# Optimization experiments

Measured on AMD Instinct MI355X. Metric: run time of the kernel, lower is better.

The kernel has to match this reference:

```python
import jax, jax.numpy as jnp
import numpy as np
import math

Ds = 2048
N = 16384
M = 1024


def setup_inputs() -> dict:
    key = jax.random.key(0)
    kD, kS, kW = jax.random.split(key, 3)
    D = jax.random.normal(kD, (N, Ds), dtype=jnp.float32)
    S = jax.random.normal(kS, (M, Ds), dtype=jnp.float32)
    W = jax.random.normal(kW, (Ds, Ds), dtype=jnp.float32) * 0.01  # init.normal std=0.01
    return {"D": D, "S": S, "W": W}


def reference(D, S, W):
    ds = D.shape[1]
    temperature = 1.0
    # cross-attention: [n, m]
    scores = (D @ S.T) / (math.sqrt(ds) * temperature)
    att_weight = jax.nn.softmax(scores, axis=1)
    att_S = att_weight @ S  # [n, Ds]
    # bilinear per row: logits[i] = D[i] . (W @ att_S[i])  -> fused einsum
    logits = jnp.einsum('nd,de,ne->n', D, W, att_S)
    log_prob = jnp.sum(jax.nn.log_sigmoid(logits))
    return log_prob
```

## Files before the change

kernel.cpp:

```cpp
#include <hip/hip_runtime.h>
#include <stdint.h>

typedef unsigned short u16;
typedef unsigned int u32;
typedef __attribute__((ext_vector_type(8))) short bf16x8;
typedef __attribute__((ext_vector_type(4))) float f32x4;

#define DS 2048
#define NROWS 16384
#define MS 1024
#define K2 2048

__device__ __forceinline__ u16 f2bf(float f) {
  u32 u = __float_as_uint(f);
  u32 r = (u + 0x7fffu + ((u >> 16) & 1u)) >> 16;
  return (u16)r;
}
__device__ __forceinline__ float bf2f(u16 h) {
  return __uint_as_float(((u32)h) << 16);
}

__global__ __launch_bounds__(256) void k_conv(const float* __restrict__ in,
                                              u16* __restrict__ out, int n4) {
  int i = blockIdx.x * blockDim.x + threadIdx.x;
  int stride = gridDim.x * blockDim.x;
  for (; i < n4; i += stride) {
    float4 v = ((const float4*)in)[i];
    ushort4 o;
    o.x = f2bf(v.x); o.y = f2bf(v.y); o.z = f2bf(v.z); o.w = f2bf(v.w);
    ((ushort4*)out)[i] = o;
  }
}

__global__ __launch_bounds__(256) void k_conv_S(const float* __restrict__ in,
                                                u16* __restrict__ Sbf,
                                                u16* __restrict__ Bt, int n4) {
  int i = blockIdx.x * blockDim.x + threadIdx.x;
  int stride = gridDim.x * blockDim.x;
  for (; i < n4; i += stride) {
    float4 v = ((const float4*)in)[i];
    ushort4 o;
    o.x = f2bf(v.x); o.y = f2bf(v.y); o.z = f2bf(v.z); o.w = f2bf(v.w);
    ((ushort4*)Sbf)[i] = o;
    int m = i >> 9;
    int c4 = i & 511;
    ((ushort4*)Bt)[(size_t)m * 1024 + c4] = o;
  }
}

__device__ __forceinline__ void gload16(const u16* g, u16* l) {
  __builtin_amdgcn_global_load_lds(
      (const __attribute__((address_space(1))) void*)g,
      (__attribute__((address_space(3))) void*)l, 16, 0, 0);
}

__global__ __launch_bounds__(256, 2) void k_gemm_bt(const u16* __restrict__ A,
                                                    const u16* __restrict__ Bt,
                                                    u16* __restrict__ C, int ldc,
                                                    int M, int N, int K) {
  __shared__ u16 lsA[128 * 32];
  __shared__ u16 lsB[128 * 32];
  const int tid = threadIdx.x;
  const int wid = tid >> 6;
  const int lane = tid & 63;
  const int brow = blockIdx.y * 128;
  const int bcol = blockIdx.x * 128;
  const int wm = wid >> 1;
  const int wn = wid & 1;

  f32x4 zero = {0.f, 0.f, 0.f, 0.f};
  f32x4 acc[4][4];
#pragma unroll
  for (int i = 0; i < 4; ++i)
#pragma unroll
    for (int j = 0; j < 4; ++j) acc[i][j] = zero;

  const int srow = lane >> 2;
  const int skoct = (lane & 3) * 8;
  const u16* gA = A + (size_t)(brow + wid * 32 + srow) * K + skoct;
  const u16* gB = Bt + (size_t)(bcol + wid * 32 + srow) * K + skoct;
  u16* lA0 = &lsA[(wid * 32) * 32];
  u16* lA1 = &lsA[(wid * 32 + 16) * 32];
  u16* lB0 = &lsB[(wid * 32) * 32];
  u16* lB1 = &lsB[(wid * 32 + 16) * 32];
  const size_t row16 = (size_t)16 * K;

  const int arow = wm * 64 + (lane & 15);
  const int bcr = wn * 64 + (lane & 15);
  const int koff = (lane >> 4) * 8;

  for (int kt = 0; kt < K; kt += 32) {
    gload16(gA + kt, lA0);
    gload16(gA + kt + row16, lA1);
    gload16(gB + kt, lB0);
    gload16(gB + kt + row16, lB1);
    __syncthreads();

    bf16x8 af[4], bfr[4];
#pragma unroll
    for (int i = 0; i < 4; ++i) af[i] = *(const bf16x8*)&lsA[(arow + i * 16) * 32 + koff];
#pragma unroll
    for (int i = 0; i < 4; ++i) bfr[i] = *(const bf16x8*)&lsB[(bcr + i * 16) * 32 + koff];
#pragma unroll
    for (int mi = 0; mi < 4; ++mi)
#pragma unroll
      for (int ni = 0; ni < 4; ++ni)
        acc[mi][ni] = __builtin_amdgcn_mfma_f32_16x16x32_bf16(af[mi], bfr[ni],
                                                              acc[mi][ni], 0, 0, 0);
    __syncthreads();
  }

  const int crow0 = brow + wm * 64 + (lane >> 4) * 4;
  const int ccol0 = bcol + wn * 64 + (lane & 15);
#pragma unroll
  for (int mi = 0; mi < 4; ++mi)
#pragma unroll
    for (int ni = 0; ni < 4; ++ni)
#pragma unroll
      for (int r = 0; r < 4; ++r)
        C[(size_t)(crow0 + mi * 16 + r) * ldc + (ccol0 + ni * 16)] = f2bf(acc[mi][ni][r]);
}

#define SINV 0.022097086912079608f

#define DSR(dst, addr) asm volatile("ds_read_b128 %0, %1" : "=v"(dst) : "v"(addr))

#define AADDR(B, QM, MI, KK) \
  ((abase + (B) * 65536u + (QM) * 16384u + (MI) * 2048u) ^ ((KK) * 64u))
#define BADDR(B, QN, NI, KK) \
  ((bbase + (B) * 65536u + (QN) * 16384u + (NI) * 2048u) ^ ((KK) * 64u))

#define STG(gptr, b, AB, h, kt)                                                     \
  do {                                                                              \
    gload16(gptr + (size_t)((h) * 128) * K2 + (kt),                                 \
            &lds[(b) * 32768 + (AB) * 16384 + (h) * 8192 + wid * 512]);             \
    gload16(gptr + (size_t)((h) * 128 + 64) * K2 + (kt),                            \
            &lds[(b) * 32768 + (AB) * 16384 + (h) * 8192 + 4096 + wid * 512]);      \
  } while (0)
#define STG_A(b, h, kt) STG(gAs, b, 0, h, kt)
#define STG_B(b, h, kt) STG(gBs, b, 1, h, kt)

#define RD_ALPHA(B)                                                   \
  do {                                                                \
    _Pragma("unroll") for (int mi = 0; mi < 4; ++mi) {                \
      DSR(af[mi][0], AADDR(B, 0, mi, 0));                             \
      DSR(af[mi][1], AADDR(B, 0, mi, 1));                             \
    }                                                                 \
    _Pragma("unroll") for (int ni = 0; ni < 2; ++ni) {                \
      DSR(bq[0][ni][0], BADDR(B, 0, ni, 0));                          \
      DSR(bq[0][ni][1], BADDR(B, 0, ni, 1));                          \
    }                                                                 \
  } while (0)
#define RD_BETA(B)                                                    \
  do {                                                                \
    _Pragma("unroll") for (int ni = 0; ni < 2; ++ni) {                \
      DSR(bq[1][ni][0], BADDR(B, 1, ni, 0));                          \
      DSR(bq[1][ni][1], BADDR(B, 1, ni, 1));                          \
    }                                                                 \
  } while (0)
#define RD_GAMMA(B)                                                   \
  do {                                                                \
    _Pragma("unroll") for (int mi = 0; mi < 4; ++mi) {                \
      DSR(af[mi][0], AADDR(B, 1, mi, 0));                             \
      DSR(af[mi][1], AADDR(B, 1, mi, 1));                             \
    }                                                                 \
  } while (0)

#define MMAQ(QM, QN)                                                               \
  do {                                                                             \
    _Pragma("unroll") for (int mi = 0; mi < 4; ++mi)                               \
        _Pragma("unroll") for (int ni = 0; ni < 2; ++ni) {                         \
      acc[QM][QN][mi][ni] = __builtin_amdgcn_mfma_f32_16x16x32_bf16(               \
          af[mi][0], bq[QN][ni][0], acc[QM][QN][mi][ni], 0, 0, 0);                 \
      acc[QM][QN][mi][ni] = __builtin_amdgcn_mfma_f32_16x16x32_bf16(               \
          af[mi][1], bq[QN][ni][1], acc[QM][QN][mi][ni], 0, 0, 0);                 \
    }                                                                              \
  } while (0)

#define PH_MID()                                              \
  __builtin_amdgcn_s_barrier();                               \
  asm volatile("s_waitcnt lgkmcnt(0)" ::: "memory");          \
  __builtin_amdgcn_sched_barrier(0);                          \
  __builtin_amdgcn_s_setprio(1)
#define PH_END() __builtin_amdgcn_s_setprio(0)
#define BAR() __builtin_amdgcn_s_barrier()
#define VM6() asm volatile("s_waitcnt vmcnt(6)" ::: "memory")
#define VM0() asm volatile("s_waitcnt vmcnt(0)" ::: "memory")

__global__ __launch_bounds__(512, 2) void k_gemm8(const u16* __restrict__ A,
                                                  const u16* __restrict__ Bt,
                                                  float* __restrict__ Pnd) {
  extern __shared__ u16 lds[];
  const int tid = threadIdx.x;
  const int wid = tid >> 6;
  const int lane = tid & 63;
  const int bid = blockIdx.x;
  const int swz = (bid & 7) * 64 + (bid >> 3);
  const int by = swz >> 3, bx = swz & 7;
  const int brow = by * 256, bcol = bx * 256;
  const int wm = wid >> 2, wn = wid & 3;
  const int l15 = lane & 15, s0 = lane >> 4;

  const int tr = tid >> 3;
  const int scol = ((tid & 7) ^ (tr & 7)) << 3;
  const u16* gAs = A + (size_t)(brow + tr) * K2 + scol;
  const u16* gBs = Bt + (size_t)(bcol + tr) * K2 + scol;

  const u32 lb = (u32)(uintptr_t)(&lds[0]);
  const u32 xorp = ((u32)(s0 ^ (lane & 7))) << 4;
  const u32 abase = lb + ((u32)(wm * 64 + l15) << 7) + xorp;
  const u32 bbase = lb + 32768u + ((u32)(wn * 32 + l15) << 7) + xorp;

  f32x4 acc[2][2][4][2];
#pragma unroll
  for (int a = 0; a < 2; ++a)
#pragma unroll
    for (int b = 0; b < 2; ++b)
#pragma unroll
      for (int c = 0; c < 4; ++c)
#pragma unroll
        for (int d = 0; d < 2; ++d) acc[a][b][c][d] = (f32x4){0.f, 0.f, 0.f, 0.f};

  bf16x8 af[4][2], bq[2][2][2];

  STG_A(0, 0, 0); STG_B(0, 0, 0); STG_B(0, 1, 0); STG_A(0, 1, 0);
  STG_A(1, 0, 64); STG_B(1, 0, 64); STG_B(1, 1, 64);
  VM6();
  BAR();

  int kt0 = 0;
#pragma unroll 1
  for (int j = 0; j < 15; ++j, kt0 += 128) {
    const int kt1 = kt0 + 64, ktn0 = kt0 + 128, ktn1 = kt0 + 192;
    RD_ALPHA(0); STG_A(1, 1, kt1);  PH_MID(); MMAQ(0, 0); PH_END(); BAR();
    RD_BETA(0);  STG_A(0, 0, ktn0); PH_MID(); MMAQ(0, 1); PH_END(); BAR();
    RD_GAMMA(0); STG_B(0, 0, ktn0); PH_MID(); MMAQ(1, 0); PH_END(); BAR();
    STG_B(0, 1, ktn0);              PH_MID(); MMAQ(1, 1); PH_END(); VM6(); BAR();
    RD_ALPHA(1); STG_A(0, 1, ktn0); PH_MID(); MMAQ(0, 0); PH_END(); BAR();
    RD_BETA(1);  STG_A(1, 0, ktn1); PH_MID(); MMAQ(0, 1); PH_END(); BAR();
    RD_GAMMA(1); STG_B(1, 0, ktn1); PH_MID(); MMAQ(1, 0); PH_END(); BAR();
    STG_B(1, 1, ktn1);              PH_MID(); MMAQ(1, 1); PH_END(); VM6(); BAR();
  }
  {
    const int kt1 = kt0 + 64;
    RD_ALPHA(0); STG_A(1, 1, kt1);  PH_MID(); MMAQ(0, 0); PH_END(); BAR();
    RD_BETA(0);                     PH_MID(); MMAQ(0, 1); PH_END(); BAR();
    RD_GAMMA(0);                    PH_MID(); MMAQ(1, 0); PH_END(); BAR();
                                    PH_MID(); MMAQ(1, 1); PH_END(); VM0(); BAR();
    RD_ALPHA(1);                    PH_MID(); MMAQ(0, 0); PH_END(); BAR();
    RD_BETA(1);                     PH_MID(); MMAQ(0, 1); PH_END(); BAR();
    RD_GAMMA(1);                    PH_MID(); MMAQ(1, 0); PH_END(); BAR();
                                    PH_MID(); MMAQ(1, 1); PH_END(); BAR();
  }

  __syncthreads();
  float* red = (float*)&lds[0];

#pragma unroll
  for (int qm = 0; qm < 2; ++qm)
#pragma unroll
    for (int mi = 0; mi < 4; ++mi)
#pragma unroll
      for (int r = 0; r < 4; ++r) {
        float num = 0.f, den = 0.f;
#pragma unroll
        for (int qn = 0; qn < 2; ++qn)
#pragma unroll
          for (int ni = 0; ni < 2; ++ni) {
            float v = acc[qm][qn][mi][ni][r];
            float g = __shfl_xor(v, 1);
            float e = __expf(v * SINV);
            num += e * g;
            den += e;
          }
        num += __shfl_xor(num, 2); den += __shfl_xor(den, 2);
        num += __shfl_xor(num, 4); den += __shfl_xor(den, 4);
        num += __shfl_xor(num, 8); den += __shfl_xor(den, 8);
        if (l15 == 0) {
          int slot = qm * 16 + mi * 4 + r;
          red[((wid * 32 + slot) * 4 + s0) * 2 + 0] = num;
          red[((wid * 32 + slot) * 4 + s0) * 2 + 1] = den;
        }
      }
  __syncthreads();
  {
    int rloc = tid >> 1, which = tid & 1;
    int qm = rloc >> 7, wmr = (rloc >> 6) & 1, mi = (rloc >> 4) & 3;
    int lg = (rloc >> 2) & 3, r = rloc & 3;
    int slot = qm * 16 + mi * 4 + r;
    float v = 0.f;
#pragma unroll
    for (int w2 = 0; w2 < 4; ++w2)
      v += red[(((wmr * 4 + w2) * 32 + slot) * 4 + lg) * 2 + which];
    Pnd[((size_t)(brow + rloc) * 8 + bx) * 2 + which] = v;
  }
}

__global__ __launch_bounds__(256) void k_rowfinal(const float* __restrict__ Pnd,
                                                  float* __restrict__ part) {
  int row = blockIdx.x * 256 + threadIdx.x;
  const float4* p = (const float4*)(Pnd + (size_t)row * 16);
  float num = 0.f, den = 0.f;
#pragma unroll
  for (int i = 0; i < 4; ++i) {
    float4 v = p[i];
    num += v.x + v.z;
    den += v.y + v.w;
  }
  float logit = num / den;
  float ls = (logit >= 0.f) ? -log1pf(__expf(-logit))
                            : (logit - log1pf(__expf(logit)));
  __shared__ float red[4];
#pragma unroll
  for (int off = 32; off > 0; off >>= 1) ls += __shfl_down(ls, off);
  if ((threadIdx.x & 63) == 0) red[threadIdx.x >> 6] = ls;
  __syncthreads();
  if (threadIdx.x == 0) part[blockIdx.x] = red[0] + red[1] + red[2] + red[3];
}

__global__ __launch_bounds__(64) void k_final64(const float* __restrict__ part,
                                                float* __restrict__ out) {
  float v = part[threadIdx.x];
#pragma unroll
  for (int off = 32; off > 0; off >>= 1) v += __shfl_down(v, off);
  if (threadIdx.x == 0) out[0] = v;
}

extern "C" void kernel_launch(void* const* d_in, const int* in_sizes, int n_in,
                              void* d_out, int out_size, void* d_ws, size_t ws_size,
                              hipStream_t stream) {
  const float* D = (const float*)d_in[0];
  const float* S = (const float*)d_in[1];
  const float* W = (const float*)d_in[2];

  char* w = (char*)d_ws;
  u16* Dbf = (u16*)w; w += (size_t)NROWS * DS * 2;
  u16* Bt = (u16*)w;  w += (size_t)DS * DS * 2;
  u16* Wbf = (u16*)w; w += (size_t)DS * DS * 2;
  u16* Sbf = (u16*)w; w += (size_t)MS * DS * 2;
  float* Pnd = (float*)w; w += (size_t)NROWS * 16 * 4;
  float* part = (float*)w;

  (void)hipFuncSetAttribute((const void*)k_gemm8,
                            hipFuncAttributeMaxDynamicSharedMemorySize, 131072);

  k_conv<<<1024, 256, 0, stream>>>(W, Wbf, DS * DS / 4);
  k_conv_S<<<512, 256, 0, stream>>>(S, Sbf, Bt, MS * DS / 4);
  k_conv<<<2048, 256, 0, stream>>>(D, Dbf, NROWS * DS / 4);

  k_gemm_bt<<<dim3(DS / 128, MS / 128), 256, 0, stream>>>(
      Sbf, Wbf, Bt + DS, 2 * DS, MS, DS, DS);

  k_gemm8<<<512, 512, 131072, stream>>>(Dbf, Bt, Pnd);

  k_rowfinal<<<NROWS / 256, 256, 0, stream>>>(Pnd, part);
  k_final64<<<1, 64, 0, stream>>>(part, (float*)d_out);
}
```

Before: 200.9 us.

## Software-pipeline LDS fragment reads in main GEMM and halve small GEMM tile rows

The main k_gemm8 loop is restructured so LDS fragment reads for the next quadrant are issued before the current MFMA batch. Double-buffered register fragments (afA/afB, bq0/bq1) and graded lgkmcnt waits replace the full lgkmcnt(0) wait each phase, so LDS latency can hide behind matrix math, and global stages are reordered with vmcnt(4) waits. Separately, the S·W GEMM uses 64-row tiles to launch twice as many blocks for better CU occupancy. The price is more fragment registers and tighter, hand-tuned wait counts that must match the issue order exactly.

```diff
diff --git a/kernel.cpp b/kernel.cpp
--- a/kernel.cpp
+++ b/kernel.cpp
@@ -54,55 +54,51 @@
       (__attribute__((address_space(3))) void*)l, 16, 0, 0);
 }
 
-__global__ __launch_bounds__(256, 2) void k_gemm_bt(const u16* __restrict__ A,
-                                                    const u16* __restrict__ Bt,
-                                                    u16* __restrict__ C, int ldc,
-                                                    int M, int N, int K) {
-  __shared__ u16 lsA[128 * 32];
+__global__ __launch_bounds__(256, 2) void k_gemm_bt64(const u16* __restrict__ A,
+                                                      const u16* __restrict__ Bt,
+                                                      u16* __restrict__ C, int ldc,
+                                                      int K) {
+  __shared__ u16 lsA[64 * 32];
   __shared__ u16 lsB[128 * 32];
   const int tid = threadIdx.x;
   const int wid = tid >> 6;
   const int lane = tid & 63;
-  const int brow = blockIdx.y * 128;
+  const int brow = blockIdx.y * 64;
   const int bcol = blockIdx.x * 128;
   const int wm = wid >> 1;
   const int wn = wid & 1;
 
-  f32x4 zero = {0.f, 0.f, 0.f, 0.f};
-  f32x4 acc[4][4];
-#pragma unroll
-  for (int i = 0; i < 4; ++i)
-#pragma unroll
-    for (int j = 0; j < 4; ++j) acc[i][j] = zero;
+  f32x4 acc[2][4];
+#pragma unroll
+  for (int i = 0; i < 2; ++i)
+#pragma unroll
+    for (int j = 0; j < 4; ++j) acc[i][j] = (f32x4){0.f, 0.f, 0.f, 0.f};
 
   const int srow = lane >> 2;
   const int skoct = (lane & 3) * 8;
-  const u16* gA = A + (size_t)(brow + wid * 32 + srow) * K + skoct;
+  const u16* gA = A + (size_t)(brow + wid * 16 + srow) * K + skoct;
   const u16* gB = Bt + (size_t)(bcol + wid * 32 + srow) * K + skoct;
-  u16* lA0 = &lsA[(wid * 32) * 32];
-  u16* lA1 = &lsA[(wid * 32 + 16) * 32];
+  u16* lA = &lsA[(wid * 16) * 32];
   u16* lB0 = &lsB[(wid * 32) * 32];
   u16* lB1 = &lsB[(wid * 32 + 16) * 32];
   const size_t row16 = (size_t)16 * K;
 
-  const int arow = wm * 64 + (lane & 15);
+  const int arow = wm * 32 + (lane & 15);
   const int bcr = wn * 64 + (lane & 15);
   const int koff = (lane >> 4) * 8;
 
   for (int kt = 0; kt < K; kt += 32) {
-    gload16(gA + kt, lA0);
-    gload16(gA + kt + row16, lA1);
+    gload16(gA + kt, lA);
     gload16(gB + kt, lB0);
     gload16(gB + kt + row16, lB1);
     __syncthreads();
-
-    bf16x8 af[4], bfr[4];
-#pragma unroll
-    for (int i = 0; i < 4; ++i) af[i] = *(const bf16x8*)&lsA[(arow + i * 16) * 32 + koff];
+    bf16x8 af[2], bfr[4];
+#pragma unroll
+    for (int i = 0; i < 2; ++i) af[i] = *(const bf16x8*)&lsA[(arow + i * 16) * 32 + koff];
 #pragma unroll
     for (int i = 0; i < 4; ++i) bfr[i] = *(const bf16x8*)&lsB[(bcr + i * 16) * 32 + koff];
 #pragma unroll
-    for (int mi = 0; mi < 4; ++mi)
+    for (int mi = 0; mi < 2; ++mi)
 #pragma unroll
       for (int ni = 0; ni < 4; ++ni)
         acc[mi][ni] = __builtin_amdgcn_mfma_f32_16x16x32_bf16(af[mi], bfr[ni],
@@ -110,10 +106,10 @@
     __syncthreads();
   }
 
-  const int crow0 = brow + wm * 64 + (lane >> 4) * 4;
+  const int crow0 = brow + wm * 32 + (lane >> 4) * 4;
   const int ccol0 = bcol + wn * 64 + (lane & 15);
 #pragma unroll
-  for (int mi = 0; mi < 4; ++mi)
+  for (int mi = 0; mi < 2; ++mi)
 #pragma unroll
     for (int ni = 0; ni < 4; ++ni)
 #pragma unroll
@@ -123,69 +119,59 @@
 
 #define SINV 0.022097086912079608f
 
-#define DSR(dst, addr) asm volatile("ds_read_b128 %0, %1" : "=v"(dst) : "v"(addr))
-
-#define AADDR(B, QM, MI, KK) \
-  ((abase + (B) * 65536u + (QM) * 16384u + (MI) * 2048u) ^ ((KK) * 64u))
-#define BADDR(B, QN, NI, KK) \
-  ((bbase + (B) * 65536u + (QN) * 16384u + (NI) * 2048u) ^ ((KK) * 64u))
-
-#define STG(gptr, b, AB, h, kt)                                                     \
-  do {                                                                              \
-    gload16(gptr + (size_t)((h) * 128) * K2 + (kt),                                 \
-            &lds[(b) * 32768 + (AB) * 16384 + (h) * 8192 + wid * 512]);             \
-    gload16(gptr + (size_t)((h) * 128 + 64) * K2 + (kt),                            \
-            &lds[(b) * 32768 + (AB) * 16384 + (h) * 8192 + 4096 + wid * 512]);      \
-  } while (0)
-#define STG_A(b, h, kt) STG(gAs, b, 0, h, kt)
-#define STG_B(b, h, kt) STG(gBs, b, 1, h, kt)
-
-#define RD_ALPHA(B)                                                   \
-  do {                                                                \
-    _Pragma("unroll") for (int mi = 0; mi < 4; ++mi) {                \
-      DSR(af[mi][0], AADDR(B, 0, mi, 0));                             \
-      DSR(af[mi][1], AADDR(B, 0, mi, 1));                             \
-    }                                                                 \
-    _Pragma("unroll") for (int ni = 0; ni < 2; ++ni) {                \
-      DSR(bq[0][ni][0], BADDR(B, 0, ni, 0));                          \
-      DSR(bq[0][ni][1], BADDR(B, 0, ni, 1));                          \
-    }                                                                 \
-  } while (0)
-#define RD_BETA(B)                                                    \
-  do {                                                                \
-    _Pragma("unroll") for (int ni = 0; ni < 2; ++ni) {                \
-      DSR(bq[1][ni][0], BADDR(B, 1, ni, 0));                          \
-      DSR(bq[1][ni][1], BADDR(B, 1, ni, 1));                          \
-    }                                                                 \
-  } while (0)
-#define RD_GAMMA(B)                                                   \
-  do {                                                                \
-    _Pragma("unroll") for (int mi = 0; mi < 4; ++mi) {                \
-      DSR(af[mi][0], AADDR(B, 1, mi, 0));                             \
-      DSR(af[mi][1], AADDR(B, 1, mi, 1));                             \
-    }                                                                 \
-  } while (0)
-
-#define MMAQ(QM, QN)                                                               \
+#define DSR(d, a, IMM) \
+  asm volatile("ds_read_b128 %0, %1 offset:%c2" : "=v"(d) : "v"(a), "n"(IMM))
+
+#define RD_A0(k0, k1, dst)                              \
+  DSR(dst[0][0], k0, 0);     DSR(dst[0][1], k1, 0);     \
+  DSR(dst[1][0], k0, 2048);  DSR(dst[1][1], k1, 2048);  \
+  DSR(dst[2][0], k0, 4096);  DSR(dst[2][1], k1, 4096);  \
+  DSR(dst[3][0], k0, 6144);  DSR(dst[3][1], k1, 6144)
+#define RD_A1(k0, k1, dst)                              \
+  DSR(dst[0][0], k0, 16384); DSR(dst[0][1], k1, 16384); \
+  DSR(dst[1][0], k0, 18432); DSR(dst[1][1], k1, 18432); \
+  DSR(dst[2][0], k0, 20480); DSR(dst[2][1], k1, 20480); \
+  DSR(dst[3][0], k0, 22528); DSR(dst[3][1], k1, 22528)
+#define RD_B0(k0, k1, dst)                              \
+  DSR(dst[0][0], k0, 0);     DSR(dst[0][1], k1, 0);     \
+  DSR(dst[1][0], k0, 2048);  DSR(dst[1][1], k1, 2048)
+#define RD_B1(k0, k1, dst)                              \
+  DSR(dst[0][0], k0, 16384); DSR(dst[0][1], k1, 16384); \
+  DSR(dst[1][0], k0, 18432); DSR(dst[1][1], k1, 18432)
+
+#define MMAQ(AF, BQ, QM, QN)                                                       \
   do {                                                                             \
     _Pragma("unroll") for (int mi = 0; mi < 4; ++mi)                               \
         _Pragma("unroll") for (int ni = 0; ni < 2; ++ni) {                         \
       acc[QM][QN][mi][ni] = __builtin_amdgcn_mfma_f32_16x16x32_bf16(               \
-          af[mi][0], bq[QN][ni][0], acc[QM][QN][mi][ni], 0, 0, 0);                 \
+          AF[mi][0], BQ[ni][0], acc[QM][QN][mi][ni], 0, 0, 0);                     \
       acc[QM][QN][mi][ni] = __builtin_amdgcn_mfma_f32_16x16x32_bf16(               \
-          af[mi][1], bq[QN][ni][1], acc[QM][QN][mi][ni], 0, 0, 0);                 \
+          AF[mi][1], BQ[ni][1], acc[QM][QN][mi][ni], 0, 0, 0);                     \
     }                                                                              \
   } while (0)
 
-#define PH_MID()                                              \
-  __builtin_amdgcn_s_barrier();                               \
-  asm volatile("s_waitcnt lgkmcnt(0)" ::: "memory");          \
-  __builtin_amdgcn_sched_barrier(0);                          \
-  __builtin_amdgcn_s_setprio(1)
-#define PH_END() __builtin_amdgcn_s_setprio(0)
+#define LGKM(N)                                              \
+  asm volatile("s_waitcnt lgkmcnt(" #N ")" ::: "memory");    \
+  __builtin_amdgcn_sched_barrier(0)
+#define VMW(N) asm volatile("s_waitcnt vmcnt(" #N ")" ::: "memory")
+#define PRIO1() __builtin_amdgcn_s_setprio(1)
+#define PRIO0() __builtin_amdgcn_s_setprio(0)
 #define BAR() __builtin_amdgcn_s_barrier()
-#define VM6() asm volatile("s_waitcnt vmcnt(6)" ::: "memory")
-#define VM0() asm volatile("s_waitcnt vmcnt(0)" ::: "memory")
+
+#define STGA(b, h, kt)                                                            \
+  do {                                                                            \
+    gload16(pA + (size_t)((h) * 128) * K2 + (kt),                                 \
+            &lds[(b) * 32768 + (h) * 8192 + wid * 512]);                          \
+    gload16(pA + (size_t)((h) * 128 + 64) * K2 + (kt),                            \
+            &lds[(b) * 32768 + (h) * 8192 + 4096 + wid * 512]);                   \
+  } while (0)
+#define STGB(b, h, kt)                                                            \
+  do {                                                                            \
+    gload16(pB + (size_t)((h) * 128) * K2 + (kt),                                 \
+            &lds[(b) * 32768 + 16384 + (h) * 8192 + wid * 512]);                  \
+    gload16(pB + (size_t)((h) * 128 + 64) * K2 + (kt),                            \
+            &lds[(b) * 32768 + 16384 + (h) * 8192 + 4096 + wid * 512]);           \
+  } while (0)
 
 __global__ __launch_bounds__(512, 2) void k_gemm8(const u16* __restrict__ A,
                                                   const u16* __restrict__ Bt,
@@ -203,13 +189,19 @@
 
   const int tr = tid >> 3;
   const int scol = ((tid & 7) ^ (tr & 7)) << 3;
-  const u16* gAs = A + (size_t)(brow + tr) * K2 + scol;
-  const u16* gBs = Bt + (size_t)(bcol + tr) * K2 + scol;
+  const u16* pA = A + (size_t)(brow + tr) * K2 + scol;
+  const u16* pB = Bt + (size_t)(bcol + tr) * K2 + scol;
 
   const u32 lb = (u32)(uintptr_t)(&lds[0]);
   const u32 xorp = ((u32)(s0 ^ (lane & 7))) << 4;
-  const u32 abase = lb + ((u32)(wm * 64 + l15) << 7) + xorp;
-  const u32 bbase = lb + 32768u + ((u32)(wn * 32 + l15) << 7) + xorp;
+  const u32 aA00 = lb + ((u32)(wm * 64 + l15) << 7) + xorp;
+  const u32 aA01 = aA00 ^ 64u;
+  const u32 aA10 = aA00 + 65536u;
+  const u32 aA11 = aA10 ^ 64u;
+  const u32 aB00 = lb + 32768u + ((u32)(wn * 32 + l15) << 7) + xorp;
+  const u32 aB01 = aB00 ^ 64u;
+  const u32 aB10 = aB00 + 65536u;
+  const u32 aB11 = aB10 ^ 64u;
 
   f32x4 acc[2][2][4][2];
 #pragma unroll
@@ -221,36 +213,61 @@
 #pragma unroll
         for (int d = 0; d < 2; ++d) acc[a][b][c][d] = (f32x4){0.f, 0.f, 0.f, 0.f};
 
-  bf16x8 af[4][2], bq[2][2][2];
-
-  STG_A(0, 0, 0); STG_B(0, 0, 0); STG_B(0, 1, 0); STG_A(0, 1, 0);
-  STG_A(1, 0, 64); STG_B(1, 0, 64); STG_B(1, 1, 64);
-  VM6();
+  bf16x8 afA[4][2], afB[4][2], bq0[2][2], bq1[2][2];
+
+  STGA(0, 0, 0); STGB(0, 0, 0); STGB(0, 1, 0); STGA(0, 1, 0);
+  STGA(1, 0, 64);
+  VMW(2);
   BAR();
-
-  int kt0 = 0;
+  RD_A0(aA00, aA01, afA);
+  RD_B0(aB00, aB01, bq0);
+
+  int kb = 0;
 #pragma unroll 1
-  for (int j = 0; j < 15; ++j, kt0 += 128) {
-    const int kt1 = kt0 + 64, ktn0 = kt0 + 128, ktn1 = kt0 + 192;
-    RD_ALPHA(0); STG_A(1, 1, kt1);  PH_MID(); MMAQ(0, 0); PH_END(); BAR();
-    RD_BETA(0);  STG_A(0, 0, ktn0); PH_MID(); MMAQ(0, 1); PH_END(); BAR();
-    RD_GAMMA(0); STG_B(0, 0, ktn0); PH_MID(); MMAQ(1, 0); PH_END(); BAR();
-    STG_B(0, 1, ktn0);              PH_MID(); MMAQ(1, 1); PH_END(); VM6(); BAR();
-    RD_ALPHA(1); STG_A(0, 1, ktn0); PH_MID(); MMAQ(0, 0); PH_END(); BAR();
-    RD_BETA(1);  STG_A(1, 0, ktn1); PH_MID(); MMAQ(0, 1); PH_END(); BAR();
-    RD_GAMMA(1); STG_B(1, 0, ktn1); PH_MID(); MMAQ(1, 0); PH_END(); BAR();
-    STG_B(1, 1, ktn1);              PH_MID(); MMAQ(1, 1); PH_END(); VM6(); BAR();
+  for (int j = 0; j < 15; ++j, kb += 128) {
+    STGB(1, 0, kb + 64);
+    RD_B1(aB00, aB01, bq1);
+    LGKM(4); PRIO1(); MMAQ(afA, bq0, 0, 0); PRIO0(); VMW(4); BAR();
+    STGB(1, 1, kb + 64);
+    RD_A1(aA00, aA01, afB);
+    LGKM(8); PRIO1(); MMAQ(afA, bq1, 0, 1); PRIO0(); VMW(4); BAR();
+    STGA(1, 1, kb + 64);
+    LGKM(0); PRIO1(); MMAQ(afB, bq0, 1, 0); PRIO0(); VMW(4); BAR();
+    STGA(0, 0, kb + 128);
+    RD_A0(aA10, aA11, afA);
+    RD_B0(aB10, aB11, bq0);
+    LGKM(12); PRIO1(); MMAQ(afB, bq1, 1, 1); PRIO0(); VMW(4); BAR();
+    STGB(0, 0, kb + 128);
+    RD_B1(aB10, aB11, bq1);
+    LGKM(4); PRIO1(); MMAQ(afA, bq0, 0, 0); PRIO0(); VMW(4); BAR();
+    STGB(0, 1, kb + 128);
+    RD_A1(aA10, aA11, afB);
+    LGKM(8); PRIO1(); MMAQ(afA, bq1, 0, 1); PRIO0(); VMW(4); BAR();
+    STGA(0, 1, kb + 128);
+    LGKM(0); PRIO1(); MMAQ(afB, bq0, 1, 0); PRIO0(); VMW(4); BAR();
+    STGA(1, 0, kb + 192);
+    RD_A0(aA00, aA01, afA);
+    RD_B0(aB00, aB01, bq0);
+    LGKM(12); PRIO1(); MMAQ(afB, bq1, 1, 1); PRIO0(); VMW(4); BAR();
   }
   {
-    const int kt1 = kt0 + 64;
-    RD_ALPHA(0); STG_A(1, 1, kt1);  PH_MID(); MMAQ(0, 0); PH_END(); BAR();
-    RD_BETA(0);                     PH_MID(); MMAQ(0, 1); PH_END(); BAR();
-    RD_GAMMA(0);                    PH_MID(); MMAQ(1, 0); PH_END(); BAR();
-                                    PH_MID(); MMAQ(1, 1); PH_END(); VM0(); BAR();
-    RD_ALPHA(1);                    PH_MID(); MMAQ(0, 0); PH_END(); BAR();
-    RD_BETA(1);                     PH_MID(); MMAQ(0, 1); PH_END(); BAR();
-    RD_GAMMA(1);                    PH_MID(); MMAQ(1, 0); PH_END(); BAR();
-                                    PH_MID(); MMAQ(1, 1); PH_END(); BAR();
+    STGB(1, 0, kb + 64);
+    RD_B1(aB00, aB01, bq1);
+    LGKM(4); PRIO1(); MMAQ(afA, bq0, 0, 0); PRIO0(); VMW(4); BAR();
+    STGB(1, 1, kb + 64);
+    RD_A1(aA00, aA01, afB);
+    LGKM(8); PRIO1(); MMAQ(afA, bq1, 0, 1); PRIO0(); VMW(4); BAR();
+    STGA(1, 1, kb + 64);
+    LGKM(0); PRIO1(); MMAQ(afB, bq0, 1, 0); PRIO0(); VMW(4); BAR();
+    RD_A0(aA10, aA11, afA);
+    RD_B0(aB10, aB11, bq0);
+    LGKM(12); PRIO1(); MMAQ(afB, bq1, 1, 1); PRIO0(); VMW(2); BAR();
+    RD_B1(aB10, aB11, bq1);
+    LGKM(4); PRIO1(); MMAQ(afA, bq0, 0, 0); PRIO0(); VMW(0); BAR();
+    RD_A1(aA10, aA11, afB);
+    LGKM(8); PRIO1(); MMAQ(afA, bq1, 0, 1); PRIO0();
+    LGKM(0); PRIO1(); MMAQ(afB, bq0, 1, 0); PRIO0();
+    MMAQ(afB, bq1, 1, 1);
   }
 
   __syncthreads();
@@ -348,8 +365,8 @@
   k_conv_S<<<512, 256, 0, stream>>>(S, Sbf, Bt, MS * DS / 4);
   k_conv<<<2048, 256, 0, stream>>>(D, Dbf, NROWS * DS / 4);
 
-  k_gemm_bt<<<dim3(DS / 128, MS / 128), 256, 0, stream>>>(
-      Sbf, Wbf, Bt + DS, 2 * DS, MS, DS, DS);
+  k_gemm_bt64<<<dim3(DS / 128, MS / 64), 256, 0, stream>>>(
+      Sbf, Wbf, Bt + DS, 2 * DS, DS);
 
   k_gemm8<<<512, 512, 131072, stream>>>(Dbf, Bt, Pnd);
 
```

New measurement: 188.7 us. -6.0%, faster.
